# Kernel tuning notes

Measured on AMD Instinct MI355X. Metric: run time of the kernel, lower is better.

## Reference

```python
import jax, jax.numpy as jnp
import numpy as np

S, B, E, H = 2048, 64, 256, 256

def setup_inputs() -> dict:
    key = jax.random.key(0)
    k1, k2, k3, k4, k5 = jax.random.split(key, 5)
    scale = 1.0 / np.sqrt(H)
    return {
        "sentence": jax.random.normal(k1, (S, B, E), dtype=jnp.float32),
        "h0": jax.random.uniform(k2, (B, H), dtype=jnp.float32),
        "W_ih": jax.random.normal(k3, (E, H), dtype=jnp.float32) * scale,
        "W_hh": jax.random.normal(k4, (H, H), dtype=jnp.float32) * scale,
        "b": jax.random.normal(k5, (H,), dtype=jnp.float32) * scale,
    }

def reference(sentence, h0, W_ih, W_hh, b):
    # Precompute input projections for all steps in one big GEMM: [S,B,H]
    x_proj = jnp.einsum("sbe,eh->sbh", sentence, W_ih) + b

    def step(h, xp):
        h_new = jnp.tanh(xp + h @ W_hh)  # [B,H]
        return h_new, None

    h_final, _ = jax.lax.scan(step, h0, x_proj)
    return h_final  # [B,H]
```

## Files before the change

### kernel.cpp

```cpp
#include <hip/hip_runtime.h>
#include <math.h>

#define S_TOT 2048
#define B_    64
#define E_    256
#define H_    256

typedef __fp16 half2v __attribute__((ext_vector_type(2)));

__device__ __forceinline__ float dpp_xor1(float x) {
    int i = __builtin_bit_cast(int, x);
    i = __builtin_amdgcn_mov_dpp(i, 0xB1, 0xF, 0xF, true);
    return __builtin_bit_cast(float, i);
}
__device__ __forceinline__ float dpp_xor2(float x) {
    int i = __builtin_bit_cast(int, x);
    i = __builtin_amdgcn_mov_dpp(i, 0x4E, 0xF, 0xF, true);
    return __builtin_bit_cast(float, i);
}

__global__ __launch_bounds__(512)
__attribute__((amdgpu_waves_per_eu(2, 2)))
void fused_step(
    const float* __restrict__ A,
    const float* __restrict__ Wih,
    const float* __restrict__ bias,
    float*       __restrict__ xp_next,
    const float* __restrict__ xp_cur,
    const float* __restrict__ Whh,
    float*       __restrict__ h,
    int steps, int scan_blocks)
{
    __shared__ float smem[32 * 68 + 32 * 64];
    const int tid = threadIdx.x;

    if ((int)blockIdx.x < scan_blocks) {
        float* hbuf = smem;
        const int b  = blockIdx.x;
        const int ks = tid & 3;
        const int jg = tid >> 2;
        const int j0 = jg << 1;
        const int jf = j0 + (ks & 1);

#define DECLW(i) int w##i##_0, w##i##_1;
        DECLW(0)  DECLW(1)  DECLW(2)  DECLW(3)  DECLW(4)  DECLW(5)  DECLW(6)  DECLW(7)
        DECLW(8)  DECLW(9)  DECLW(10) DECLW(11) DECLW(12) DECLW(13) DECLW(14) DECLW(15)
        DECLW(16) DECLW(17) DECLW(18) DECLW(19) DECLW(20) DECLW(21) DECLW(22) DECLW(23)
        DECLW(24) DECLW(25) DECLW(26) DECLW(27) DECLW(28) DECLW(29) DECLW(30) DECLW(31)

#define LOADW(i) { \
        const float* r0_ = &Whh[(size_t)(ks * 64 + 2 * i) * H_ + j0]; \
        const float* r1_ = r0_ + H_; \
        half2v v0_ = __builtin_amdgcn_cvt_pkrtz(r0_[0], r1_[0]); \
        half2v v1_ = __builtin_amdgcn_cvt_pkrtz(r0_[1], r1_[1]); \
        w##i##_0 = __builtin_bit_cast(int, v0_); \
        w##i##_1 = __builtin_bit_cast(int, v1_); \
        asm volatile("" : "+v"(w##i##_0), "+v"(w##i##_1)); \
    }
        LOADW(0)  LOADW(1)  LOADW(2)  LOADW(3)  LOADW(4)  LOADW(5)  LOADW(6)  LOADW(7)
        LOADW(8)  LOADW(9)  LOADW(10) LOADW(11) LOADW(12) LOADW(13) LOADW(14) LOADW(15)
        LOADW(16) LOADW(17) LOADW(18) LOADW(19) LOADW(20) LOADW(21) LOADW(22) LOADW(23)
        LOADW(24) LOADW(25) LOADW(26) LOADW(27) LOADW(28) LOADW(29) LOADW(30) LOADW(31)

        if (tid < 128) {
            half2v hp = __builtin_amdgcn_cvt_pkrtz(h[b * H_ + 2 * tid],
                                                   h[b * H_ + 2 * tid + 1]);
            ((half2v*)hbuf)[(tid >> 5) * 36 + (tid & 31)] = hp;
        }
        float xpn = xp_cur[(size_t)b * H_ + jf];
        __syncthreads();

        int p = 0;
        const int rd_base = ks * 36;
        const int wr_idx  = (jg >> 5) * 36 + (jg & 31);
        for (int s = 0; s < steps; s++) {
            const float xpc = xpn;
            if (s + 1 < steps)
                xpn = xp_cur[((size_t)(s + 1) * B_ + b) * H_ + jf];

            half2v hk[32];
            {
                const float4* hs = (const float4*)&hbuf[p * 144 + rd_base];
                #pragma unroll
                for (int t = 0; t < 8; t++)
                    *(float4*)&hk[t * 4] = hs[t];
            }

            float p00 = 0.f, p01 = 0.f, p10 = 0.f, p11 = 0.f;
#define DOTA(i) \
            p00 = __builtin_amdgcn_fdot2(hk[i], __builtin_bit_cast(half2v, w##i##_0), p00, false); \
            p01 = __builtin_amdgcn_fdot2(hk[i], __builtin_bit_cast(half2v, w##i##_1), p01, false);
#define DOTB(i) \
            p10 = __builtin_amdgcn_fdot2(hk[i], __builtin_bit_cast(half2v, w##i##_0), p10, false); \
            p11 = __builtin_amdgcn_fdot2(hk[i], __builtin_bit_cast(half2v, w##i##_1), p11, false);
            DOTA(0)  DOTA(1)  DOTA(2)  DOTA(3)  DOTA(4)  DOTA(5)  DOTA(6)  DOTA(7)
            DOTA(8)  DOTA(9)  DOTA(10) DOTA(11) DOTA(12) DOTA(13) DOTA(14) DOTA(15)
            DOTB(16) DOTB(17) DOTB(18) DOTB(19) DOTB(20) DOTB(21) DOTB(22) DOTB(23)
            DOTB(24) DOTB(25) DOTB(26) DOTB(27) DOTB(28) DOTB(29) DOTB(30) DOTB(31)

            const float acc0 = p00 + p10;
            const float acc1 = p01 + p11;

            const bool b0 = (ks & 1);
            const float r = (b0 ? acc1 : acc0) + dpp_xor1(b0 ? acc0 : acc1);
            const float v = r + dpp_xor2(r) + xpc;

            const float e2 = __expf(2.f * v);
            const float hn = 1.f - 2.f / (e2 + 1.f);

            const float other = dpp_xor1(hn);
            if (ks == 0) {
                ((half2v*)hbuf)[(p ^ 1) * 144 + wr_idx] =
                    __builtin_amdgcn_cvt_pkrtz(hn, other);
                if (s == steps - 1) {
                    float2 o; o.x = hn; o.y = other;
                    *(float2*)&h[b * H_ + j0] = o;
                }
            }
            __syncthreads();
            p ^= 1;
        }
    } else if (A != nullptr) {
        float (*As)[68] = (float(*)[68])smem;
        float (*Bs)[64] = (float(*)[64])(smem + 32 * 68);

        const int gid = blockIdx.x - scan_blocks;
        const int bm = (gid >> 2) * 64;
        const int bn = (gid & 3) * 64;
        const int tx = tid & 15;
        const int ty = tid >> 4;

        float acc[2][4] = {};

        const int ar = tid >> 3;
        const int ak = (tid & 7) << 2;
        const int br = tid >> 4;
        const int bc = (tid & 15) << 2;

        for (int k0 = 0; k0 < E_; k0 += 32) {
            float4 a0  = *(const float4*)&A[(size_t)(bm + ar) * E_ + k0 + ak];
            float4 bv0 = *(const float4*)&Wih[(size_t)(k0 + br) * H_ + bn + bc];

            As[ak+0][ar] = a0.x; As[ak+1][ar] = a0.y;
            As[ak+2][ar] = a0.z; As[ak+3][ar] = a0.w;
            *(float4*)&Bs[br][bc] = bv0;
            __syncthreads();

            #pragma unroll
            for (int kk = 0; kk < 32; kk++) {
                const float2 av = *(const float2*)&As[kk][ty << 1];
                const float4 bv = *(const float4*)&Bs[kk][tx << 2];
                acc[0][0] += av.x*bv.x; acc[0][1] += av.x*bv.y;
                acc[0][2] += av.x*bv.z; acc[0][3] += av.x*bv.w;
                acc[1][0] += av.y*bv.x; acc[1][1] += av.y*bv.y;
                acc[1][2] += av.y*bv.z; acc[1][3] += av.y*bv.w;
            }
            __syncthreads();
        }

        const float4 bb = *(const float4*)&bias[bn + (tx << 2)];
        #pragma unroll
        for (int i = 0; i < 2; i++) {
            float4 o;
            o.x = acc[i][0] + bb.x;
            o.y = acc[i][1] + bb.y;
            o.z = acc[i][2] + bb.z;
            o.w = acc[i][3] + bb.w;
            *(float4*)&xp_next[(size_t)(bm + (ty << 1) + i) * H_ + bn + (tx << 2)] = o;
        }
    }
}

extern "C" void kernel_launch(void* const* d_in, const int* in_sizes, int n_in,
                              void* d_out, int out_size, void* d_ws, size_t ws_size,
                              hipStream_t stream)
{
    const float* sentence = (const float*)d_in[0];
    const float* h0       = (const float*)d_in[1];
    const float* W_ih     = (const float*)d_in[2];
    const float* W_hh     = (const float*)d_in[3];
    const float* bias     = (const float*)d_in[4];
    float* h  = (float*)d_out;
    float* ws = (float*)d_ws;

    int chunk = 256;
    while ((size_t)2 * chunk * B_ * H_ * sizeof(float) > ws_size && chunk > 32)
        chunk >>= 1;
    const int nchunk = S_TOT / chunk;
    float* buf[2] = { ws, ws + (size_t)chunk * B_ * H_ };

    hipMemcpyAsync(h, h0, B_ * H_ * sizeof(float), hipMemcpyDeviceToDevice, stream);

    fused_step<<<chunk * 4, 512, 0, stream>>>(sentence, W_ih, bias, buf[0],
                                              nullptr, W_hh, h, 0, 0);
    for (int c = 0; c < nchunk; c++) {
        const bool last = (c == nchunk - 1);
        const int gemmb = last ? 0 : chunk * 4;
        const float* Anext = last ? nullptr
                                  : sentence + (size_t)(c + 1) * chunk * B_ * E_;
        fused_step<<<64 + gemmb, 512, 0, stream>>>(Anext, W_ih, bias,
                                                   buf[(c + 1) & 1],
                                                   buf[c & 1], W_hh, h,
                                                   chunk, 64);
    }
}
```

Before: 1.338 ms.

## Halve block size, give each scan thread four output columns and double GEMM tile

Scan blocks now use 256 threads, each holding weights for four hidden columns (128 packed fp16 registers) instead of two. Reductions and the h writeback are reworked with DPP swaps to match. The GEMM blocks compute a 4x4 micro-tile per thread with doubled loads so the tile size stays the same. The goal is fewer waves taking part in each per-step __syncthreads and less reduction overhead per output. The cost is higher register pressure at one wave per EU and less latency hiding.

```diff
diff --git a/kernel.cpp b/kernel.cpp
--- a/kernel.cpp
+++ b/kernel.cpp
@@ -18,9 +18,15 @@
     i = __builtin_amdgcn_mov_dpp(i, 0x4E, 0xF, 0xF, true);
     return __builtin_bit_cast(float, i);
 }
-
-__global__ __launch_bounds__(512)
-__attribute__((amdgpu_waves_per_eu(2, 2)))
+__device__ __forceinline__ int dpp_xor1_i(int i) {
+    return __builtin_amdgcn_mov_dpp(i, 0xB1, 0xF, 0xF, true);
+}
+__device__ __forceinline__ int dpp_xor2_i(int i) {
+    return __builtin_amdgcn_mov_dpp(i, 0x4E, 0xF, 0xF, true);
+}
+
+__global__ __launch_bounds__(256)
+__attribute__((amdgpu_waves_per_eu(1, 1)))
 void fused_step(
     const float* __restrict__ A,
     const float* __restrict__ Wih,
@@ -39,10 +45,10 @@
         const int b  = blockIdx.x;
         const int ks = tid & 3;
         const int jg = tid >> 2;
-        const int j0 = jg << 1;
-        const int jf = j0 + (ks & 1);
-
-#define DECLW(i) int w##i##_0, w##i##_1;
+        const int j0 = jg << 2;
+        const int jf = j0 + ((ks & 1) << 1) + ((ks >> 1) & 1);
+
+#define DECLW(i) int w##i##_0, w##i##_1, w##i##_2, w##i##_3;
         DECLW(0)  DECLW(1)  DECLW(2)  DECLW(3)  DECLW(4)  DECLW(5)  DECLW(6)  DECLW(7)
         DECLW(8)  DECLW(9)  DECLW(10) DECLW(11) DECLW(12) DECLW(13) DECLW(14) DECLW(15)
         DECLW(16) DECLW(17) DECLW(18) DECLW(19) DECLW(20) DECLW(21) DECLW(22) DECLW(23)
@@ -53,9 +59,14 @@
         const float* r1_ = r0_ + H_; \
         half2v v0_ = __builtin_amdgcn_cvt_pkrtz(r0_[0], r1_[0]); \
         half2v v1_ = __builtin_amdgcn_cvt_pkrtz(r0_[1], r1_[1]); \
+        half2v v2_ = __builtin_amdgcn_cvt_pkrtz(r0_[2], r1_[2]); \
+        half2v v3_ = __builtin_amdgcn_cvt_pkrtz(r0_[3], r1_[3]); \
         w##i##_0 = __builtin_bit_cast(int, v0_); \
         w##i##_1 = __builtin_bit_cast(int, v1_); \
-        asm volatile("" : "+v"(w##i##_0), "+v"(w##i##_1)); \
+        w##i##_2 = __builtin_bit_cast(int, v2_); \
+        w##i##_3 = __builtin_bit_cast(int, v3_); \
+        asm volatile("" : "+v"(w##i##_0), "+v"(w##i##_1), \
+                          "+v"(w##i##_2), "+v"(w##i##_3)); \
     }
         LOADW(0)  LOADW(1)  LOADW(2)  LOADW(3)  LOADW(4)  LOADW(5)  LOADW(6)  LOADW(7)
         LOADW(8)  LOADW(9)  LOADW(10) LOADW(11) LOADW(12) LOADW(13) LOADW(14) LOADW(15)
@@ -72,7 +83,7 @@
 
         int p = 0;
         const int rd_base = ks * 36;
-        const int wr_idx  = (jg >> 5) * 36 + (jg & 31);
+        const int wr_idx  = (jg >> 4) * 36 + ((jg & 15) << 1);
         for (int s = 0; s < steps; s++) {
             const float xpc = xpn;
             if (s + 1 < steps)
@@ -86,37 +97,57 @@
                     *(float4*)&hk[t * 4] = hs[t];
             }
 
-            float p00 = 0.f, p01 = 0.f, p10 = 0.f, p11 = 0.f;
+            float pA0 = 0.f, pA1 = 0.f, pA2 = 0.f, pA3 = 0.f;
+            float pB0 = 0.f, pB1 = 0.f, pB2 = 0.f, pB3 = 0.f;
 #define DOTA(i) \
-            p00 = __builtin_amdgcn_fdot2(hk[i], __builtin_bit_cast(half2v, w##i##_0), p00, false); \
-            p01 = __builtin_amdgcn_fdot2(hk[i], __builtin_bit_cast(half2v, w##i##_1), p01, false);
+            pA0 = __builtin_amdgcn_fdot2(hk[i], __builtin_bit_cast(half2v, w##i##_0), pA0, false); \
+            pA1 = __builtin_amdgcn_fdot2(hk[i], __builtin_bit_cast(half2v, w##i##_1), pA1, false); \
+            pA2 = __builtin_amdgcn_fdot2(hk[i], __builtin_bit_cast(half2v, w##i##_2), pA2, false); \
+            pA3 = __builtin_amdgcn_fdot2(hk[i], __builtin_bit_cast(half2v, w##i##_3), pA3, false);
 #define DOTB(i) \
-            p10 = __builtin_amdgcn_fdot2(hk[i], __builtin_bit_cast(half2v, w##i##_0), p10, false); \
-            p11 = __builtin_amdgcn_fdot2(hk[i], __builtin_bit_cast(half2v, w##i##_1), p11, false);
+            pB0 = __builtin_amdgcn_fdot2(hk[i], __builtin_bit_cast(half2v, w##i##_0), pB0, false); \
+            pB1 = __builtin_amdgcn_fdot2(hk[i], __builtin_bit_cast(half2v, w##i##_1), pB1, false); \
+            pB2 = __builtin_amdgcn_fdot2(hk[i], __builtin_bit_cast(half2v, w##i##_2), pB2, false); \
+            pB3 = __builtin_amdgcn_fdot2(hk[i], __builtin_bit_cast(half2v, w##i##_3), pB3, false);
             DOTA(0)  DOTA(1)  DOTA(2)  DOTA(3)  DOTA(4)  DOTA(5)  DOTA(6)  DOTA(7)
             DOTA(8)  DOTA(9)  DOTA(10) DOTA(11) DOTA(12) DOTA(13) DOTA(14) DOTA(15)
             DOTB(16) DOTB(17) DOTB(18) DOTB(19) DOTB(20) DOTB(21) DOTB(22) DOTB(23)
             DOTB(24) DOTB(25) DOTB(26) DOTB(27) DOTB(28) DOTB(29) DOTB(30) DOTB(31)
 
-            const float acc0 = p00 + p10;
-            const float acc1 = p01 + p11;
-
-            const bool b0 = (ks & 1);
-            const float r = (b0 ? acc1 : acc0) + dpp_xor1(b0 ? acc0 : acc1);
-            const float v = r + dpp_xor2(r) + xpc;
+            const float acc0 = pA0 + pB0;
+            const float acc1 = pA1 + pB1;
+            const float acc2 = pA2 + pB2;
+            const float acc3 = pA3 + pB3;
+
+            const bool b0 = (ks & 1), b1 = (ks & 2);
+            float r0, r1;
+            {
+                float s0 = b0 ? acc0 : acc2;
+                float s1 = b0 ? acc1 : acc3;
+                r0 = (b0 ? acc2 : acc0) + dpp_xor1(s0);
+                r1 = (b0 ? acc3 : acc1) + dpp_xor1(s1);
+            }
+            float q;
+            {
+                float s2 = b1 ? r0 : r1;
+                q = (b1 ? r1 : r0) + dpp_xor2(s2);
+            }
+            const float v = q + xpc;
 
             const float e2 = __expf(2.f * v);
             const float hn = 1.f - 2.f / (e2 + 1.f);
 
-            const float other = dpp_xor1(hn);
+            const float from2 = dpp_xor2(hn);
+            half2v pk = __builtin_amdgcn_cvt_pkrtz(hn, from2);
+            int pki = __builtin_bit_cast(int, pk);
+            int slotB = dpp_xor1_i(pki);
             if (ks == 0) {
-                ((half2v*)hbuf)[(p ^ 1) * 144 + wr_idx] =
-                    __builtin_amdgcn_cvt_pkrtz(hn, other);
-                if (s == steps - 1) {
-                    float2 o; o.x = hn; o.y = other;
-                    *(float2*)&h[b * H_ + j0] = o;
-                }
-            }
+                float2 wv;
+                wv.x = __builtin_bit_cast(float, pki);
+                wv.y = __builtin_bit_cast(float, slotB);
+                *(float2*)&((half2v*)hbuf)[(p ^ 1) * 144 + wr_idx] = wv;
+            }
+            if (s == steps - 1) h[b * H_ + jf] = hn;
             __syncthreads();
             p ^= 1;
         }
@@ -130,7 +161,7 @@
         const int tx = tid & 15;
         const int ty = tid >> 4;
 
-        float acc[2][4] = {};
+        float acc[4][4] = {};
 
         const int ar = tid >> 3;
         const int ak = (tid & 7) << 2;
@@ -138,35 +169,38 @@
         const int bc = (tid & 15) << 2;
 
         for (int k0 = 0; k0 < E_; k0 += 32) {
-            float4 a0  = *(const float4*)&A[(size_t)(bm + ar) * E_ + k0 + ak];
-            float4 bv0 = *(const float4*)&Wih[(size_t)(k0 + br) * H_ + bn + bc];
-
-            As[ak+0][ar] = a0.x; As[ak+1][ar] = a0.y;
-            As[ak+2][ar] = a0.z; As[ak+3][ar] = a0.w;
-            *(float4*)&Bs[br][bc] = bv0;
+            float4 a0 = *(const float4*)&A[(size_t)(bm + ar)      * E_ + k0 + ak];
+            float4 a1 = *(const float4*)&A[(size_t)(bm + ar + 32) * E_ + k0 + ak];
+            float4 bv0 = *(const float4*)&Wih[(size_t)(k0 + br)      * H_ + bn + bc];
+            float4 bv1 = *(const float4*)&Wih[(size_t)(k0 + br + 16) * H_ + bn + bc];
+
+            As[ak+0][ar]    = a0.x; As[ak+1][ar]    = a0.y; As[ak+2][ar]    = a0.z; As[ak+3][ar]    = a0.w;
+            As[ak+0][ar+32] = a1.x; As[ak+1][ar+32] = a1.y; As[ak+2][ar+32] = a1.z; As[ak+3][ar+32] = a1.w;
+            *(float4*)&Bs[br][bc]      = bv0;
+            *(float4*)&Bs[br + 16][bc] = bv1;
             __syncthreads();
 
             #pragma unroll
             for (int kk = 0; kk < 32; kk++) {
-                const float2 av = *(const float2*)&As[kk][ty << 1];
+                const float4 av = *(const float4*)&As[kk][ty << 2];
                 const float4 bv = *(const float4*)&Bs[kk][tx << 2];
-                acc[0][0] += av.x*bv.x; acc[0][1] += av.x*bv.y;
-                acc[0][2] += av.x*bv.z; acc[0][3] += av.x*bv.w;
-                acc[1][0] += av.y*bv.x; acc[1][1] += av.y*bv.y;
-                acc[1][2] += av.y*bv.z; acc[1][3] += av.y*bv.w;
+                acc[0][0] += av.x*bv.x; acc[0][1] += av.x*bv.y; acc[0][2] += av.x*bv.z; acc[0][3] += av.x*bv.w;
+                acc[1][0] += av.y*bv.x; acc[1][1] += av.y*bv.y; acc[1][2] += av.y*bv.z; acc[1][3] += av.y*bv.w;
+                acc[2][0] += av.z*bv.x; acc[2][1] += av.z*bv.y; acc[2][2] += av.z*bv.z; acc[2][3] += av.z*bv.w;
+                acc[3][0] += av.w*bv.x; acc[3][1] += av.w*bv.y; acc[3][2] += av.w*bv.z; acc[3][3] += av.w*bv.w;
             }
             __syncthreads();
         }
 
         const float4 bb = *(const float4*)&bias[bn + (tx << 2)];
         #pragma unroll
-        for (int i = 0; i < 2; i++) {
+        for (int i = 0; i < 4; i++) {
             float4 o;
             o.x = acc[i][0] + bb.x;
             o.y = acc[i][1] + bb.y;
             o.z = acc[i][2] + bb.z;
             o.w = acc[i][3] + bb.w;
-            *(float4*)&xp_next[(size_t)(bm + (ty << 1) + i) * H_ + bn + (tx << 2)] = o;
+            *(float4*)&xp_next[(size_t)(bm + (ty << 2) + i) * H_ + bn + (tx << 2)] = o;
         }
     }
 }
@@ -191,14 +225,14 @@
 
     hipMemcpyAsync(h, h0, B_ * H_ * sizeof(float), hipMemcpyDeviceToDevice, stream);
 
-    fused_step<<<chunk * 4, 512, 0, stream>>>(sentence, W_ih, bias, buf[0],
+    fused_step<<<chunk * 4, 256, 0, stream>>>(sentence, W_ih, bias, buf[0],
                                               nullptr, W_hh, h, 0, 0);
     for (int c = 0; c < nchunk; c++) {
         const bool last = (c == nchunk - 1);
         const int gemmb = last ? 0 : chunk * 4;
         const float* Anext = last ? nullptr
                                   : sentence + (size_t)(c + 1) * chunk * B_ * E_;
-        fused_step<<<64 + gemmb, 512, 0, stream>>>(Anext, W_ih, bias,
+        fused_step<<<64 + gemmb, 256, 0, stream>>>(Anext, W_ih, bias,
                                                    buf[(c + 1) & 1],
                                                    buf[c & 1], W_hh, h,
                                                    chunk, 64);
```

Measured after the change: 1.213 ms. 1.1x faster.
